# Kernel optimization log

Measured on AMD Instinct MI355X. Metric: run time of the kernel, lower is better.

## Reference

```python
import jax, jax.numpy as jnp
import numpy as np

D = 256        # node/edge feature dim
H = 256        # MLP hidden dim
NG = 80000     # grid (src) nodes
NM = 20000     # mesh (dst) nodes
E = 160000     # g2m edges
EPS = 1e-5


def _mlp(x, W1, b1, W2, b2, g, beta):
    # MeshGraphMLP with hidden_layers=1: Linear -> SiLU -> Linear -> LayerNorm
    h = jax.nn.silu(x @ W1 + b1)
    y = h @ W2 + b2
    mu = jnp.mean(y, axis=-1, keepdims=True)
    var = jnp.var(y, axis=-1, keepdims=True)
    return (y - mu) * jax.lax.rsqrt(var + EPS) * g + beta


def setup_inputs() -> dict:
    key = jax.random.key(0)
    ks = jax.random.split(key, 16)

    def rn(k, shape, s=0.02):
        return jax.random.normal(k, shape, dtype=jnp.float32) * s

    inp = {
        "g2m_efeat": jax.random.normal(ks[0], (E, D), dtype=jnp.float32),
        "grid_nfeat": jax.random.normal(ks[1], (NG, D), dtype=jnp.float32),
        "mesh_nfeat": jax.random.normal(ks[2], (NM, D), dtype=jnp.float32),
        "src_idx": jax.random.randint(ks[3], (E,), 0, NG, dtype=jnp.int32),
        "dst_idx": jax.random.randint(ks[4], (E,), 0, NM, dtype=jnp.int32),
        # edge MLP (concat variant): input = [efeat | src_feat | dst_feat] -> 3D
        "eW1": rn(ks[5], (3 * D, H)), "eb1": jnp.zeros((H,), jnp.float32),
        "eW2": rn(ks[6], (H, D)),     "eb2": jnp.zeros((D,), jnp.float32),
        "eg": jnp.ones((D,), jnp.float32), "ebeta": jnp.zeros((D,), jnp.float32),
        # src node MLP: D -> H -> D
        "sW1": rn(ks[7], (D, H)), "sb1": jnp.zeros((H,), jnp.float32),
        "sW2": rn(ks[8], (H, D)), "sb2": jnp.zeros((D,), jnp.float32),
        "sg": jnp.ones((D,), jnp.float32), "sbeta": jnp.zeros((D,), jnp.float32),
        # dst node MLP: (D_agg + D_node) = 2D -> H -> D
        "dW1": rn(ks[9], (2 * D, H)), "db1": jnp.zeros((H,), jnp.float32),
        "dW2": rn(ks[10], (H, D)),    "db2": jnp.zeros((D,), jnp.float32),
        "dg": jnp.ones((D,), jnp.float32), "dbeta": jnp.zeros((D,), jnp.float32),
    }
    return inp


def reference(g2m_efeat, grid_nfeat, mesh_nfeat, src_idx, dst_idx,
              eW1, eb1, eW2, eb2, eg, ebeta,
              sW1, sb1, sW2, sb2, sg, sbeta,
              dW1, db1, dW2, db2, dg, dbeta):
    # edge MLP: gather src/dst node features, concat with edge features
    e_in = jnp.concatenate(
        [g2m_efeat, grid_nfeat[src_idx], mesh_nfeat[dst_idx]], axis=-1)  # [E, 3D]
    efeat = _mlp(e_in, eW1, eb1, eW2, eb2, eg, ebeta)                    # [E, D]
    # aggregate_and_concat: copy_e_sum scatter to dst mesh nodes, concat node feats
    agg = jax.ops.segment_sum(efeat, dst_idx, num_segments=NM)           # [NM, D]
    cat_feat = jnp.concatenate([agg, mesh_nfeat], axis=-1)               # [NM, 2D]
    mesh_out = mesh_nfeat + _mlp(cat_feat, dW1, db1, dW2, db2, dg, dbeta)
    grid_out = grid_nfeat + _mlp(grid_nfeat, sW1, sb1, sW2, sb2, sg, sbeta)
    return (grid_out, mesh_out)
```

## Files before the change

### kernel.cpp

```cpp
#include <hip/hip_runtime.h>
#include <hip/hip_bf16.h>

#define DD 256
#define NGN 80000
#define NMN 20000
#define NEE 160000

typedef unsigned short u16;
typedef __attribute__((ext_vector_type(8))) short s16x8;
typedef __attribute__((ext_vector_type(4))) short s16x4;
typedef __attribute__((ext_vector_type(4))) float f32x4;

__device__ __forceinline__ u16 f2bf(float f) {
  __hip_bfloat16 h = __float2bfloat16(f);
  union { __hip_bfloat16 h; u16 u; } v; v.h = h;
  return v.u;
}
__device__ __forceinline__ float bf2f(u16 x) {
  union { unsigned u; float f; } v; v.u = ((unsigned)x) << 16;
  return v.f;
}
__device__ __forceinline__ float silu(float x) {
  return x * __builtin_amdgcn_rcpf(1.f + __expf(-x));
}

__device__ __forceinline__ s16x8 ldsA(const u16* uni, int rowL, int cL) {
  int swz = (rowL & 7) << 4;
  s16x4 lo = *(const s16x4*)((const char*)uni + rowL * 512 + ((cL * 2) ^ swz));
  s16x4 hi = *(const s16x4*)((const char*)uni + rowL * 512 + (((cL + 16) * 2) ^ swz));
  s16x8 a;
#pragma unroll
  for (int j = 0; j < 4; ++j) { a[j] = lo[j]; a[4 + j] = hi[j]; }
  return a;
}

__global__ void pack_hist(const float* __restrict__ eW1, const float* __restrict__ eW2,
                          const float* __restrict__ sW1, const float* __restrict__ sW2,
                          const float* __restrict__ dW1, const float* __restrict__ dW2,
                          u16* __restrict__ wp, const int* __restrict__ didx,
                          int* __restrict__ cnt) {
  int bid = blockIdx.x;
  if (bid < 2304) {
    const float* W; u16* dst; int lb;
    if (bid < 768)       { W = eW1; dst = wp;              lb = bid; }
    else if (bid < 1024) { W = eW2; dst = wp + 768 * 256;  lb = bid - 768; }
    else if (bid < 1280) { W = sW1; dst = wp + 1024 * 256; lb = bid - 1024; }
    else if (bid < 1536) { W = sW2; dst = wp + 1280 * 256; lb = bid - 1280; }
    else if (bid < 2048) { W = dW1; dst = wp + 1536 * 256; lb = bid - 1536; }
    else                 { W = dW2; dst = wp + 2048 * 256; lb = bid - 2048; }
    int idx = lb * 256 + threadIdx.x;
    int i = idx & 7, lane = (idx >> 3) & 63, nt = (idx >> 9) & 15, kt = idx >> 13;
    int k = kt * 32 + 4 * (lane >> 4) + (i < 4 ? i : 12 + i);
    int n = nt * 16 + (lane & 15);
    dst[idx] = f2bf(W[(size_t)k * 256 + n]);
  } else {
    int i = (bid - 2304) * 256 + threadIdx.x;
    if (i < NEE) atomicAdd(cnt + didx[i], 1);
  }
}

__global__ void csr_scan(const int* __restrict__ cnt, int* __restrict__ cursor) {
  __shared__ int psum[256];
  const int CH = (NMN + 255) / 256;
  int t = threadIdx.x;
  int base = t * CH, s = 0;
  for (int k = 0; k < CH; ++k) { int i = base + k; if (i < NMN) s += cnt[i]; }
  psum[t] = s;
  __syncthreads();
  for (int off = 1; off < 256; off <<= 1) {
    int v = (t >= off) ? psum[t - off] : 0;
    __syncthreads();
    psum[t] += v;
    __syncthreads();
  }
  int run = psum[t] - s;
  for (int k = 0; k < CH; ++k) {
    int i = base + k;
    if (i < NMN) { cursor[i] = run; run += cnt[i]; }
  }
}

__device__ __forceinline__ void gemm_body(u16* uni, const float* __restrict__ X,
                                          const u16* __restrict__ Wp, u16* __restrict__ Y,
                                          int n, int blk) {
  const int tid = threadIdx.x;
  const int lane = tid & 63;
  const int wave = tid >> 6;
  const int mr = wave >> 1, nc = wave & 1;
  const int g = lane >> 4, lr = lane & 15;
  const int row0 = blk * 64;

#pragma unroll
  for (int j = 0; j < 8; ++j) {
    int e = wave * 16 + j * 2 + (lane >> 5);
    int r = min(row0 + e, n - 1);
    const float* src = X + (size_t)r * DD + (lane & 31) * 8;
    f32x4 f0 = *(const f32x4*)src;
    f32x4 f1 = *(const f32x4*)(src + 4);
    s16x8 o;
#pragma unroll
    for (int k = 0; k < 4; ++k) { o[k] = (short)f2bf(f0[k]); o[4 + k] = (short)f2bf(f1[k]); }
    int co = (lane & 31) * 8;
    *(s16x8*)((char*)uni + e * 512 + ((co * 2) ^ ((e & 7) << 4))) = o;
  }
  __syncthreads();

  const f32x4 fz = {0.f, 0.f, 0.f, 0.f};
  f32x4 acc[2][8];
#pragma unroll
  for (int mt = 0; mt < 2; ++mt)
#pragma unroll
    for (int nt = 0; nt < 8; ++nt) acc[mt][nt] = fz;

  for (int kl = 0; kl < 8; ++kl) {
    s16x8 afr[2];
#pragma unroll
    for (int mt = 0; mt < 2; ++mt) afr[mt] = ldsA(uni, mr * 32 + mt * 16 + lr, kl * 32 + 4 * g);
#pragma unroll
    for (int h = 0; h < 2; ++h) {
      s16x8 bfr[4];
#pragma unroll
      for (int q = 0; q < 4; ++q)
        bfr[q] = *(const s16x8*)(Wp + (size_t)kl * 8192 + ((nc * 8 + h * 4 + q) * 64 + lane) * 8);
#pragma unroll
      for (int q = 0; q < 4; ++q) {
        acc[0][h * 4 + q] = __builtin_amdgcn_mfma_f32_16x16x32_bf16(afr[0], bfr[q], acc[0][h * 4 + q], 0, 0, 0);
        acc[1][h * 4 + q] = __builtin_amdgcn_mfma_f32_16x16x32_bf16(afr[1], bfr[q], acc[1][h * 4 + q], 0, 0, 0);
      }
    }
  }
  __syncthreads();
#pragma unroll
  for (int mt = 0; mt < 2; ++mt)
#pragma unroll
    for (int nt = 0; nt < 8; ++nt)
#pragma unroll
      for (int i = 0; i < 4; ++i) {
        int rowL = mr * 32 + mt * 16 + 4 * g + i;
        int col = nc * 128 + nt * 16 + lr;
        *(u16*)((char*)uni + rowL * 512 + ((col * 2) ^ ((rowL & 7) << 4))) = f2bf(acc[mt][nt][i]);
      }
  __syncthreads();
#pragma unroll
  for (int rr = 0; rr < 16; ++rr) {
    int rowL = wave * 16 + rr;
    int rg = row0 + rowL;
    if (rg < n) {
      s16x4 v = *(const s16x4*)((char*)uni + rowL * 512 + ((lane * 8) ^ ((rowL & 7) << 4)));
      *(s16x4*)(Y + (size_t)rg * DD + lane * 4) = v;
    }
  }
}

__global__ __launch_bounds__(256, 3) void gemm_fill(
    const float* __restrict__ efeat, const float* __restrict__ gridf,
    const float* __restrict__ mesh, const u16* __restrict__ wp,
    u16* __restrict__ ECp, u16* __restrict__ GSp, u16* __restrict__ GMp,
    const int* __restrict__ didx, int* __restrict__ cursor, int* __restrict__ eids) {
  __shared__ u16 uni[16384];
  int bid = blockIdx.x;
  if (bid < 2500) gemm_body(uni, efeat, wp, ECp, NEE, bid);
  else if (bid < 3750) gemm_body(uni, gridf, wp + 8 * 8192, GSp, NGN, bid - 2500);
  else if (bid < 4063) gemm_body(uni, mesh, wp + 16 * 8192, GMp, NMN, bid - 3750);
  else {
    int e = (bid - 4063) * 256 + threadIdx.x;
    if (e < NEE) { int p = atomicAdd(cursor + didx[e], 1); eids[p] = e; }
  }
}

template <int MODE, int K1>
__device__ __forceinline__ void mlp_body(
    u16* uni, float2 (*pstats)[2],
    const float* __restrict__ xa, const float* __restrict__ xb,
    const u16* __restrict__ W1p, const float* __restrict__ b1,
    const u16* __restrict__ W2p, const float* __restrict__ b2,
    const float* __restrict__ gam, const float* __restrict__ bet,
    const float* __restrict__ resid, float* __restrict__ out, int nrows, int blk) {
  const int tid = threadIdx.x;
  const int lane = tid & 63;
  const int wave = tid >> 6;
  const int mr = wave >> 1, nc = wave & 1;
  const int g = lane >> 4, lr = lane & 15;
  const int row0 = blk * 64;

  const f32x4 fz = {0.f, 0.f, 0.f, 0.f};
  f32x4 acc[2][8];
#pragma unroll
  for (int mt = 0; mt < 2; ++mt)
#pragma unroll
    for (int nt = 0; nt < 8; ++nt) acc[mt][nt] = fz;

#pragma unroll
  for (int region = 0; region < K1 / 256; ++region) {
    __syncthreads();
    const float* Xr = (region == 0) ? xa : xb;
#pragma unroll
    for (int j = 0; j < 8; ++j) {
      int e = wave * 16 + j * 2 + (lane >> 5);
      int r = min(row0 + e, nrows - 1);
      const float* src = Xr + (size_t)r * DD + (lane & 31) * 8;
      f32x4 f0 = *(const f32x4*)src;
      f32x4 f1 = *(const f32x4*)(src + 4);
      s16x8 o;
#pragma unroll
      for (int k = 0; k < 4; ++k) { o[k] = (short)f2bf(f0[k]); o[4 + k] = (short)f2bf(f1[k]); }
      int co = (lane & 31) * 8;
      *(s16x8*)((char*)uni + e * 512 + ((co * 2) ^ ((e & 7) << 4))) = o;
    }
    __syncthreads();
    for (int kl = 0; kl < 8; ++kl) {
      const int kt = region * 8 + kl;
      s16x8 afr[2];
#pragma unroll
      for (int mt = 0; mt < 2; ++mt) afr[mt] = ldsA(uni, mr * 32 + mt * 16 + lr, kl * 32 + 4 * g);
#pragma unroll
      for (int h = 0; h < 2; ++h) {
        s16x8 bfr[4];
#pragma unroll
        for (int q = 0; q < 4; ++q)
          bfr[q] = *(const s16x8*)(W1p + (size_t)kt * 8192 + ((nc * 8 + h * 4 + q) * 64 + lane) * 8);
#pragma unroll
        for (int q = 0; q < 4; ++q) {
          acc[0][h * 4 + q] = __builtin_amdgcn_mfma_f32_16x16x32_bf16(afr[0], bfr[q], acc[0][h * 4 + q], 0, 0, 0);
          acc[1][h * 4 + q] = __builtin_amdgcn_mfma_f32_16x16x32_bf16(afr[1], bfr[q], acc[1][h * 4 + q], 0, 0, 0);
        }
      }
    }
  }
  __syncthreads();

  {
    float b1v[8];
#pragma unroll
    for (int nt = 0; nt < 8; ++nt) b1v[nt] = b1[nc * 128 + nt * 16 + lr];
#pragma unroll
    for (int mt = 0; mt < 2; ++mt)
#pragma unroll
      for (int nt = 0; nt < 8; ++nt)
#pragma unroll
        for (int i = 0; i < 4; ++i) {
          float x = acc[mt][nt][i] + b1v[nt];
          float h = silu(x);
          int rowL = mr * 32 + mt * 16 + 4 * g + i;
          int col = nc * 128 + nt * 16 + lr;
          *(u16*)((char*)uni + rowL * 512 + ((col * 2) ^ ((rowL & 7) << 4))) = f2bf(h);
        }
  }
  __syncthreads();

#pragma unroll
  for (int mt = 0; mt < 2; ++mt)
#pragma unroll
    for (int nt = 0; nt < 8; ++nt) acc[mt][nt] = fz;
  for (int kl = 0; kl < 8; ++kl) {
    s16x8 afr[2];
#pragma unroll
    for (int mt = 0; mt < 2; ++mt) afr[mt] = ldsA(uni, mr * 32 + mt * 16 + lr, kl * 32 + 4 * g);
#pragma unroll
    for (int h = 0; h < 2; ++h) {
      s16x8 bfr[4];
#pragma unroll
      for (int q = 0; q < 4; ++q)
        bfr[q] = *(const s16x8*)(W2p + (size_t)kl * 8192 + ((nc * 8 + h * 4 + q) * 64 + lane) * 8);
#pragma unroll
      for (int q = 0; q < 4; ++q) {
        acc[0][h * 4 + q] = __builtin_amdgcn_mfma_f32_16x16x32_bf16(afr[0], bfr[q], acc[0][h * 4 + q], 0, 0, 0);
        acc[1][h * 4 + q] = __builtin_amdgcn_mfma_f32_16x16x32_bf16(afr[1], bfr[q], acc[1][h * 4 + q], 0, 0, 0);
      }
    }
  }

  float b2v[8], gv[8], bv[8];
#pragma unroll
  for (int nt = 0; nt < 8; ++nt) {
    int col = nc * 128 + nt * 16 + lr;
    b2v[nt] = b2[col];
    gv[nt] = gam[col];
    bv[nt] = bet[col];
  }
#pragma unroll
  for (int mt = 0; mt < 2; ++mt)
#pragma unroll
    for (int i = 0; i < 4; ++i) {
      float s = 0.f, s2 = 0.f;
#pragma unroll
      for (int nt = 0; nt < 8; ++nt) {
        float y = acc[mt][nt][i] + b2v[nt];
        s += y;
        s2 += y * y;
      }
#pragma unroll
      for (int m = 1; m < 16; m <<= 1) {
        s += __shfl_xor(s, m);
        s2 += __shfl_xor(s2, m);
      }
      if (lr == 0) pstats[mr * 32 + mt * 16 + 4 * g + i][nc] = make_float2(s, s2);
    }
  __syncthreads();
#pragma unroll
  for (int mt = 0; mt < 2; ++mt)
#pragma unroll
    for (int i = 0; i < 4; ++i) {
      int rowL = mr * 32 + mt * 16 + 4 * g + i;
      float2 pa = pstats[rowL][0], pb = pstats[rowL][1];
      float sum = pa.x + pb.x, sq = pa.y + pb.y;
      float mu = sum * (1.f / 256.f);
      float var = fmaxf(sq * (1.f / 256.f) - mu * mu, 0.f);
      float rs = rsqrtf(var + 1e-5f);
      int rg = row0 + rowL;
      if (MODE == 2 && rg >= nrows) continue;
#pragma unroll
      for (int nt = 0; nt < 8; ++nt) {
        int col = nc * 128 + nt * 16 + lr;
        float y = acc[mt][nt][i] + b2v[nt];
        float val = (y - mu) * rs * gv[nt] + bv[nt];
        out[(size_t)rg * DD + col] = resid[(size_t)rg * DD + col] + val;
      }
    }
}

__device__ __forceinline__ void edge_body(
    u16* uni, float2 (*pstats)[2], int* eidL, int* srcL, int* dstL,
    const u16* __restrict__ ECp, const u16* __restrict__ GSp, const u16* __restrict__ GMp,
    const int* __restrict__ sidx, const int* __restrict__ eids,
    const float* __restrict__ b1,
    const u16* __restrict__ W2p, const float* __restrict__ b2,
    const float* __restrict__ gam, const float* __restrict__ bet,
    const int* __restrict__ didx, float* __restrict__ agg, int blk) {
  const int tid = threadIdx.x;
  const int lane = tid & 63;
  const int wave = tid >> 6;
  const int mr = wave >> 1, nc = wave & 1;
  const int g = lane >> 4, lr = lane & 15;
  const int row0 = blk * 64;

  if (tid < 64) {
    int e = eids[row0 + tid];
    eidL[tid] = e;
    srcL[tid] = sidx[e];
    dstL[tid] = didx[e];
  }
  __syncthreads();

  const int co = (lane & 31) * 8;
  f32x4 b1a = *(const f32x4*)(b1 + co);
  f32x4 b1b = *(const f32x4*)(b1 + co + 4);
#pragma unroll
  for (int j = 0; j < 8; ++j) {
    int e = wave * 16 + j * 2 + (lane >> 5);
    s16x8 va = *(const s16x8*)(ECp + (size_t)eidL[e] * DD + co);
    s16x8 vb = *(const s16x8*)(GSp + (size_t)srcL[e] * DD + co);
    s16x8 vc = *(const s16x8*)(GMp + (size_t)dstL[e] * DD + co);
    s16x8 o;
#pragma unroll
    for (int k = 0; k < 8; ++k) {
      float bk = (k < 4) ? b1a[k] : b1b[k - 4];
      float x = bf2f((u16)va[k]) + bf2f((u16)vb[k]) + bf2f((u16)vc[k]) + bk;
      o[k] = (short)f2bf(silu(x));
    }
    *(s16x8*)((char*)uni + e * 512 + ((co * 2) ^ ((e & 7) << 4))) = o;
  }
  __syncthreads();

  const f32x4 fz = {0.f, 0.f, 0.f, 0.f};
  f32x4 acc[2][8];
#pragma unroll
  for (int mt = 0; mt < 2; ++mt)
#pragma unroll
    for (int nt = 0; nt < 8; ++nt) acc[mt][nt] = fz;
  for (int kl = 0; kl < 8; ++kl) {
    s16x8 afr[2];
#pragma unroll
    for (int mt = 0; mt < 2; ++mt) afr[mt] = ldsA(uni, mr * 32 + mt * 16 + lr, kl * 32 + 4 * g);
#pragma unroll
    for (int h = 0; h < 2; ++h) {
      s16x8 bfr[4];
#pragma unroll
      for (int q = 0; q < 4; ++q)
        bfr[q] = *(const s16x8*)(W2p + (size_t)kl * 8192 + ((nc * 8 + h * 4 + q) * 64 + lane) * 8);
#pragma unroll
      for (int q = 0; q < 4; ++q) {
        acc[0][h * 4 + q] = __builtin_amdgcn_mfma_f32_16x16x32_bf16(afr[0], bfr[q], acc[0][h * 4 + q], 0, 0, 0);
        acc[1][h * 4 + q] = __builtin_amdgcn_mfma_f32_16x16x32_bf16(afr[1], bfr[q], acc[1][h * 4 + q], 0, 0, 0);
      }
    }
  }

  float b2v[8], gv[8], bv[8];
#pragma unroll
  for (int nt = 0; nt < 8; ++nt) {
    int col = nc * 128 + nt * 16 + lr;
    b2v[nt] = b2[col];
    gv[nt] = gam[col];
    bv[nt] = bet[col];
  }
#pragma unroll
  for (int mt = 0; mt < 2; ++mt)
#pragma unroll
    for (int i = 0; i < 4; ++i) {
      float s = 0.f, s2 = 0.f;
#pragma unroll
      for (int nt = 0; nt < 8; ++nt) {
        float y = acc[mt][nt][i] + b2v[nt];
        s += y;
        s2 += y * y;
      }
#pragma unroll
      for (int m = 1; m < 16; m <<= 1) {
        s += __shfl_xor(s, m);
        s2 += __shfl_xor(s2, m);
      }
      if (lr == 0) pstats[mr * 32 + mt * 16 + 4 * g + i][nc] = make_float2(s, s2);
    }
  __syncthreads();

#pragma unroll
  for (int mt = 0; mt < 2; ++mt)
#pragma unroll
    for (int i = 0; i < 4; ++i) {
      int rowL = mr * 32 + mt * 16 + 4 * g + i;
      float2 pa = pstats[rowL][0], pb = pstats[rowL][1];
      float sum = pa.x + pb.x, sq = pa.y + pb.y;
      float mu = sum * (1.f / 256.f);
      float var = fmaxf(sq * (1.f / 256.f) - mu * mu, 0.f);
      float rs = rsqrtf(var + 1e-5f);
#pragma unroll
      for (int nt = 0; nt < 8; ++nt) {
        int col = nc * 128 + nt * 16 + lr;
        float y = acc[mt][nt][i] + b2v[nt];
        float val = (y - mu) * rs * gv[nt] + bv[nt];
        *(u16*)((char*)uni + rowL * 512 + ((col * 2) ^ ((rowL & 7) << 4))) = f2bf(val);
      }
    }
  __syncthreads();

  {
    int c = tid;
    float sum = 0.f;
    int prev = dstL[0];
#pragma unroll 8
    for (int r = 0; r < 64; ++r) {
      int d = dstL[r];
      if (d != prev) {
        atomicAdd(agg + (size_t)prev * DD + c, sum);
        sum = 0.f;
        prev = d;
      }
      sum += bf2f(*(const u16*)((char*)uni + r * 512 + ((c * 2) ^ ((r & 7) << 4))));
    }
    atomicAdd(agg + (size_t)prev * DD + c, sum);
  }
}

__global__ __launch_bounds__(256, 3) void edge_mlp(
    const u16* __restrict__ ECp, const u16* __restrict__ GSp, const u16* __restrict__ GMp,
    const int* __restrict__ sidx, const int* __restrict__ eids,
    const float* __restrict__ eb1,
    const u16* __restrict__ eW2p, const float* __restrict__ eb2,
    const float* __restrict__ eg, const float* __restrict__ ebt,
    const int* __restrict__ didx, float* __restrict__ agg,
    const float* __restrict__ gridf,
    const u16* __restrict__ sW1p, const float* __restrict__ sb1,
    const u16* __restrict__ sW2p, const float* __restrict__ sb2,
    const float* __restrict__ sg, const float* __restrict__ sbt,
    float* __restrict__ gout, int withMlp) {
  __shared__ u16 uni[16384];
  __shared__ float2 pstats[64][2];
  __shared__ int eidL[64], srcL[64], dstL[64];
  int bid = blockIdx.x;
  if (withMlp) {
    if ((bid % 3) == 2) {
      mlp_body<1, 256>(uni, pstats, gridf, nullptr, sW1p, sb1, sW2p, sb2,
                       sg, sbt, gridf, gout, NGN, bid / 3);
      return;
    }
    bid = (bid / 3) * 2 + (bid % 3);
  }
  edge_body(uni, pstats, eidL, srcL, dstL, ECp, GSp, GMp, sidx, eids,
            eb1, eW2p, eb2, eg, ebt, didx, agg, bid);
}

__global__ __launch_bounds__(256, 3) void mlp12_kernel(
    const float* __restrict__ agg, const float* __restrict__ mesh,
    const u16* __restrict__ dW1p, const float* __restrict__ db1,
    const u16* __restrict__ dW2p, const float* __restrict__ db2,
    const float* __restrict__ dg, const float* __restrict__ dbt,
    float* __restrict__ mout,
    const float* __restrict__ gridf,
    const u16* __restrict__ sW1p, const float* __restrict__ sb1,
    const u16* __restrict__ sW2p, const float* __restrict__ sb2,
    const float* __restrict__ sg, const float* __restrict__ sbt,
    float* __restrict__ gout, int withMlp1) {
  __shared__ u16 uni[16384];
  __shared__ float2 pstats[64][2];
  int bid = blockIdx.x;
  if (bid < 313) {
    mlp_body<2, 512>(uni, pstats, agg, mesh, dW1p, db1, dW2p, db2, dg, dbt,
                     mesh, mout, NMN, bid);
  } else if (withMlp1) {
    mlp_body<1, 256>(uni, pstats, gridf, nullptr, sW1p, sb1, sW2p, sb2,
                     sg, sbt, gridf, gout, NGN, bid - 313);
  }
}

extern "C" void kernel_launch(void* const* d_in, const int* in_sizes, int n_in,
                              void* d_out, int out_size, void* d_ws, size_t ws_size,
                              hipStream_t stream) {
  const float* g2m  = (const float*)d_in[0];
  const float* grid = (const float*)d_in[1];
  const float* mesh = (const float*)d_in[2];
  const int* sidx = (const int*)d_in[3];
  const int* didx = (const int*)d_in[4];
  const float* eW1 = (const float*)d_in[5];
  const float* eb1 = (const float*)d_in[6];
  const float* eW2 = (const float*)d_in[7];
  const float* eb2 = (const float*)d_in[8];
  const float* eg  = (const float*)d_in[9];
  const float* ebt = (const float*)d_in[10];
  const float* sW1 = (const float*)d_in[11];
  const float* sb1 = (const float*)d_in[12];
  const float* sW2 = (const float*)d_in[13];
  const float* sb2 = (const float*)d_in[14];
  const float* sg  = (const float*)d_in[15];
  const float* sbt = (const float*)d_in[16];
  const float* dW1 = (const float*)d_in[17];
  const float* db1 = (const float*)d_in[18];
  const float* dW2 = (const float*)d_in[19];
  const float* db2 = (const float*)d_in[20];
  const float* dg  = (const float*)d_in[21];
  const float* dbt = (const float*)d_in[22];

  char* w = (char*)d_ws;
  float* agg = (float*)w;
  u16* wp = (u16*)(w + 20480000);
  int* cnt = (int*)(w + 20480000 + 1179648);
  int* cursor = cnt + 20480;
  int* eids = cursor + 20480;
  const size_t GS_OFF = 22463488;
  const size_t EC_OFF = GS_OFF + (size_t)NGN * DD * 2 + (size_t)NMN * DD * 2;
  const size_t NEED_BIG = EC_OFF + (size_t)NEE * DD * 2;

  u16* eW1p = wp;
  u16* eW2p = eW1p + 768 * 256;
  u16* sW1p = eW2p + 256 * 256;
  u16* sW2p = sW1p + 256 * 256;
  u16* dW1p = sW2p + 256 * 256;
  u16* dW2p = dW1p + 512 * 256;

  float* gout = (float*)d_out;
  float* mout = gout + (size_t)NGN * DD;

  u16* GSp = (u16*)(w + GS_OFF);
  u16* GMp = GSp + (size_t)NGN * DD;
  const bool big = ws_size >= NEED_BIG;
  u16* ECp = big ? (u16*)(w + EC_OFF) : (u16*)d_out;

  (void)hipMemsetAsync(agg, 0, 20480000, stream);
  (void)hipMemsetAsync(cnt, 0, 81920, stream);

  pack_hist<<<2304 + 625, 256, 0, stream>>>(eW1, eW2, sW1, sW2, dW1, dW2, wp, didx, cnt);
  csr_scan<<<1, 256, 0, stream>>>(cnt, cursor);
  gemm_fill<<<4063 + 625, 256, 0, stream>>>(g2m, grid, mesh, wp, ECp, GSp, GMp,
                                            didx, cursor, eids);

  if (big) {
    edge_mlp<<<3750, 256, 0, stream>>>(
        ECp, GSp, GMp, sidx, eids, eb1, eW2p, eb2, eg, ebt, didx, agg,
        grid, sW1p, sb1, sW2p, sb2, sg, sbt, gout, 1);
    mlp12_kernel<<<313, 256, 0, stream>>>(
        agg, mesh, dW1p, db1, dW2p, db2, dg, dbt, mout,
        grid, sW1p, sb1, sW2p, sb2, sg, sbt, gout, 0);
  } else {
    edge_mlp<<<2500, 256, 0, stream>>>(
        ECp, GSp, GMp, sidx, eids, eb1, eW2p, eb2, eg, ebt, didx, agg,
        grid, sW1p, sb1, sW2p, sb2, sg, sbt, gout, 0);
    mlp12_kernel<<<313 + 1250, 256, 0, stream>>>(
        agg, mesh, dW1p, db1, dW2p, db2, dg, dbt, mout,
        grid, sW1p, sb1, sW2p, sb2, sg, sbt, gout, 1);
  }
}
```

Before: 369.8 us.

## Move grid node MLP from edge kernel into gemm_fill launch

The grid (src) node MLP blocks were interleaved with the edge MLP blocks. They now run interleaved with the edge-feature projection GEMM blocks inside gemm_fill, and the edge kernel becomes a dedicated launch. This rebalances work so the heavy gathered edge kernel is not shared with MLP blocks, and the node MLP overlaps the bandwidth-bound projection stage instead. It increases gemm_fill grid size and register/LDS pressure in that kernel, and the mlp weight offsets into the packed buffer are now hardcoded.

```diff
diff --git a/kernel.cpp b/kernel.cpp
--- a/kernel.cpp
+++ b/kernel.cpp
@@ -152,22 +152,6 @@
   }
 }
 
-__global__ __launch_bounds__(256, 3) void gemm_fill(
-    const float* __restrict__ efeat, const float* __restrict__ gridf,
-    const float* __restrict__ mesh, const u16* __restrict__ wp,
-    u16* __restrict__ ECp, u16* __restrict__ GSp, u16* __restrict__ GMp,
-    const int* __restrict__ didx, int* __restrict__ cursor, int* __restrict__ eids) {
-  __shared__ u16 uni[16384];
-  int bid = blockIdx.x;
-  if (bid < 2500) gemm_body(uni, efeat, wp, ECp, NEE, bid);
-  else if (bid < 3750) gemm_body(uni, gridf, wp + 8 * 8192, GSp, NGN, bid - 2500);
-  else if (bid < 4063) gemm_body(uni, mesh, wp + 16 * 8192, GMp, NMN, bid - 3750);
-  else {
-    int e = (bid - 4063) * 256 + threadIdx.x;
-    if (e < NEE) { int p = atomicAdd(cursor + didx[e], 1); eids[p] = e; }
-  }
-}
-
 template <int MODE, int K1>
 __device__ __forceinline__ void mlp_body(
     u16* uni, float2 (*pstats)[2],
@@ -319,20 +303,55 @@
     }
 }
 
-__device__ __forceinline__ void edge_body(
-    u16* uni, float2 (*pstats)[2], int* eidL, int* srcL, int* dstL,
+__global__ __launch_bounds__(256, 3) void gemm_fill(
+    const float* __restrict__ efeat, const float* __restrict__ gridf,
+    const float* __restrict__ mesh, const u16* __restrict__ wp,
+    u16* __restrict__ ECp, u16* __restrict__ GSp, u16* __restrict__ GMp,
+    const int* __restrict__ didx, int* __restrict__ cursor, int* __restrict__ eids,
+    const float* __restrict__ sb1, const float* __restrict__ sb2,
+    const float* __restrict__ sg, const float* __restrict__ sbt,
+    float* __restrict__ gout, int withMlp) {
+  __shared__ u16 uni[16384];
+  __shared__ float2 pstats[64][2];
+  int bid = blockIdx.x;
+  if (withMlp) {
+    if (bid < 3750) {
+      if ((bid % 3) == 2) {
+        mlp_body<1, 256>(uni, pstats, gridf, nullptr, wp + 1024 * 256, sb1,
+                         wp + 1280 * 256, sb2, sg, sbt, gridf, gout, NGN, bid / 3);
+        return;
+      }
+      gemm_body(uni, efeat, wp, ECp, NEE, (bid / 3) * 2 + (bid % 3));
+      return;
+    }
+    bid -= 1250;
+  }
+  if (bid < 2500) gemm_body(uni, efeat, wp, ECp, NEE, bid);
+  else if (bid < 3750) gemm_body(uni, gridf, wp + 8 * 8192, GSp, NGN, bid - 2500);
+  else if (bid < 4063) gemm_body(uni, mesh, wp + 16 * 8192, GMp, NMN, bid - 3750);
+  else {
+    int e = (bid - 4063) * 256 + threadIdx.x;
+    if (e < NEE) { int p = atomicAdd(cursor + didx[e], 1); eids[p] = e; }
+  }
+}
+
+__global__ __launch_bounds__(256, 3) void edge_kern(
     const u16* __restrict__ ECp, const u16* __restrict__ GSp, const u16* __restrict__ GMp,
     const int* __restrict__ sidx, const int* __restrict__ eids,
     const float* __restrict__ b1,
     const u16* __restrict__ W2p, const float* __restrict__ b2,
     const float* __restrict__ gam, const float* __restrict__ bet,
-    const int* __restrict__ didx, float* __restrict__ agg, int blk) {
+    const int* __restrict__ didx, float* __restrict__ agg) {
+  __shared__ u16 uni[16384];
+  __shared__ float2 pstats[64][2];
+  __shared__ int eidL[64], srcL[64], dstL[64];
+
   const int tid = threadIdx.x;
   const int lane = tid & 63;
   const int wave = tid >> 6;
   const int mr = wave >> 1, nc = wave & 1;
   const int g = lane >> 4, lr = lane & 15;
-  const int row0 = blk * 64;
+  const int row0 = blockIdx.x * 64;
 
   if (tid < 64) {
     int e = eids[row0 + tid];
@@ -450,34 +469,6 @@
     }
     atomicAdd(agg + (size_t)prev * DD + c, sum);
   }
-}
-
-__global__ __launch_bounds__(256, 3) void edge_mlp(
-    const u16* __restrict__ ECp, const u16* __restrict__ GSp, const u16* __restrict__ GMp,
-    const int* __restrict__ sidx, const int* __restrict__ eids,
-    const float* __restrict__ eb1,
-    const u16* __restrict__ eW2p, const float* __restrict__ eb2,
-    const float* __restrict__ eg, const float* __restrict__ ebt,
-    const int* __restrict__ didx, float* __restrict__ agg,
-    const float* __restrict__ gridf,
-    const u16* __restrict__ sW1p, const float* __restrict__ sb1,
-    const u16* __restrict__ sW2p, const float* __restrict__ sb2,
-    const float* __restrict__ sg, const float* __restrict__ sbt,
-    float* __restrict__ gout, int withMlp) {
-  __shared__ u16 uni[16384];
-  __shared__ float2 pstats[64][2];
-  __shared__ int eidL[64], srcL[64], dstL[64];
-  int bid = blockIdx.x;
-  if (withMlp) {
-    if ((bid % 3) == 2) {
-      mlp_body<1, 256>(uni, pstats, gridf, nullptr, sW1p, sb1, sW2p, sb2,
-                       sg, sbt, gridf, gout, NGN, bid / 3);
-      return;
-    }
-    bid = (bid / 3) * 2 + (bid % 3);
-  }
-  edge_body(uni, pstats, eidL, srcL, dstL, ECp, GSp, GMp, sidx, eids,
-            eb1, eW2p, eb2, eg, ebt, didx, agg, bid);
 }
 
 __global__ __launch_bounds__(256, 3) void mlp12_kernel(
@@ -560,20 +551,22 @@
 
   pack_hist<<<2304 + 625, 256, 0, stream>>>(eW1, eW2, sW1, sW2, dW1, dW2, wp, didx, cnt);
   csr_scan<<<1, 256, 0, stream>>>(cnt, cursor);
-  gemm_fill<<<4063 + 625, 256, 0, stream>>>(g2m, grid, mesh, wp, ECp, GSp, GMp,
-                                            didx, cursor, eids);
 
   if (big) {
-    edge_mlp<<<3750, 256, 0, stream>>>(
-        ECp, GSp, GMp, sidx, eids, eb1, eW2p, eb2, eg, ebt, didx, agg,
-        grid, sW1p, sb1, sW2p, sb2, sg, sbt, gout, 1);
+    gemm_fill<<<5938, 256, 0, stream>>>(g2m, grid, mesh, wp, ECp, GSp, GMp,
+                                        didx, cursor, eids,
+                                        sb1, sb2, sg, sbt, gout, 1);
+    edge_kern<<<2500, 256, 0, stream>>>(
+        ECp, GSp, GMp, sidx, eids, eb1, eW2p, eb2, eg, ebt, didx, agg);
     mlp12_kernel<<<313, 256, 0, stream>>>(
         agg, mesh, dW1p, db1, dW2p, db2, dg, dbt, mout,
         grid, sW1p, sb1, sW2p, sb2, sg, sbt, gout, 0);
   } else {
-    edge_mlp<<<2500, 256, 0, stream>>>(
-        ECp, GSp, GMp, sidx, eids, eb1, eW2p, eb2, eg, ebt, didx, agg,
-        grid, sW1p, sb1, sW2p, sb2, sg, sbt, gout, 0);
+    gemm_fill<<<4688, 256, 0, stream>>>(g2m, grid, mesh, wp, ECp, GSp, GMp,
+                                        didx, cursor, eids,
+                                        sb1, sb2, sg, sbt, gout, 0);
+    edge_kern<<<2500, 256, 0, stream>>>(
+        ECp, GSp, GMp, sidx, eids, eb1, eW2p, eb2, eg, ebt, didx, agg);
     mlp12_kernel<<<313 + 1250, 256, 0, stream>>>(
         agg, mesh, dW1p, db1, dW2p, db2, dg, dbt, mout,
         grid, sW1p, sb1, sW2p, sb2, sg, sbt, gout, 1);
```

New measurement: 362.2 us. 2.1% less time.
